# Performance work log

Hardware: AMD Instinct MI355X
Metric: run time of the kernel (lower is better)

## Reference

```python
import jax, jax.numpy as jnp
import numpy as np

B, S, D, H, L = 32, 1024, 512, 8, 4
DH = D // H
FF = D            # dim_feedforward == hidden_dim in the original ctor call
LOC_D, TD_D = 16, 8
TD_EMB = 3        # time_dist_embed_dim
POI = 21          # poi vocab
POI_EMB = 3
ADDR_IN = 1 + POI_EMB
FC = 32           # fc_hidden_dim
NEG = -1e9


def setup_inputs() -> dict:
    key = jax.random.key(0)
    ks = jax.random.split(key, 20)
    g = lambda i, shape, s=0.02: jax.random.normal(ks[i], shape, jnp.float32) * s
    return {
        "addr": jax.random.normal(ks[0], (B, 1), jnp.float32),
        "loc_dense_seq": jax.random.normal(ks[1], (B, S, LOC_D), jnp.float32),
        "time_dist_seq": jax.random.normal(ks[2], (B, S, TD_D), jnp.float32),
        "Wtd": g(3, (TD_D, TD_EMB)), "btd": jnp.zeros((TD_EMB,), jnp.float32),
        "Wemb": g(4, (LOC_D + TD_EMB, D)), "bemb": jnp.zeros((D,), jnp.float32),
        "Wqkv": g(5, (L, D, 3 * D)), "bqkv": jnp.zeros((L, 3 * D), jnp.float32),
        "Wo": g(6, (L, D, D)), "bo": jnp.zeros((L, D), jnp.float32),
        "ln1_g": jnp.ones((L, D), jnp.float32), "ln1_b": jnp.zeros((L, D), jnp.float32),
        "W1": g(7, (L, D, FF)), "b1": jnp.zeros((L, FF), jnp.float32),
        "W2": g(8, (L, FF, D)), "b2": jnp.zeros((L, D), jnp.float32),
        "ln2_g": jnp.ones((L, D), jnp.float32), "ln2_b": jnp.zeros((L, D), jnp.float32),
        "poi_emb": g(9, (POI, POI_EMB), 1.0),
        "Wa": g(10, (ADDR_IN, FC)), "ba": jnp.zeros((FC,), jnp.float32),
        "Wout": g(11, (D, FC)),
        "Wcomb": g(12, (FC, 1)),
        "addr_type": jax.random.randint(ks[13], (B, 1), 0, POI),
        "data_length": jax.random.randint(ks[14], (B,), 1, S + 1),
    }


def _ln(x, g, b, eps=1e-5):
    m = x.mean(-1, keepdims=True)
    v = ((x - m) ** 2).mean(-1, keepdims=True)
    return (x - m) / jnp.sqrt(v + eps) * g + b


def reference(addr, loc_dense_seq, time_dist_seq, Wtd, btd, Wemb, bemb, Wqkv,
              bqkv, Wo, bo, ln1_g, ln1_b, W1, b1, W2, b2, ln2_g, ln2_b,
              poi_emb, Wa, ba, Wout, Wcomb, addr_type, data_length):
    valid = jnp.arange(S)[None, :] < data_length[:, None]            # [B,S]
    td = time_dist_seq @ Wtd + btd                                   # [B,S,3]
    x = jnp.concatenate([loc_dense_seq, td], axis=-1) @ Wemb + bemb  # [B,S,D]
    scale = 1.0 / jnp.sqrt(jnp.float32(DH))
    for l in range(L):  # post-norm TransformerEncoderLayer (relu, eval/no-dropout)
        qkv = x @ Wqkv[l] + bqkv[l]
        q, k, v = jnp.split(qkv, 3, axis=-1)
        q = q.reshape(B, S, H, DH)
        k = k.reshape(B, S, H, DH)
        v = v.reshape(B, S, H, DH)
        scores = jnp.einsum('bqhd,bkhd->bhqk', q, k) * scale
        scores = jnp.where(valid[:, None, None, :], scores, NEG)     # mask padded keys
        attn = jax.nn.softmax(scores, axis=-1)
        ctx = jnp.einsum('bhqk,bkhd->bqhd', attn, v).reshape(B, S, D)
        x = _ln(x + ctx @ Wo[l] + bo[l], ln1_g[l], ln1_b[l])
        ff = jax.nn.relu(x @ W1[l] + b1[l]) @ W2[l] + b2[l]
        x = _ln(x + ff, ln2_g[l], ln2_b[l])
    # per-sample addr branch (vectorized over the original python loop)
    addr_inp = jnp.concatenate([addr, poi_emb[addr_type[:, 0]]], axis=-1)  # [B,4]
    a = addr_inp @ Wa + ba                                                 # [B,FC]
    o = (jnp.tanh(x @ Wout + a[:, None, :]) @ Wcomb)[..., 0]              # [B,S]
    logits = jnp.where(valid, o, NEG)
    logp = jax.nn.log_softmax(logits, axis=1)  # log_softmax over valid positions only
    return jnp.where(valid, logp, 0.0)
```

## Files before the change

kernel.cpp:

```cpp
#include <hip/hip_runtime.h>
#include <stdint.h>


typedef unsigned short u16;
typedef __attribute__((ext_vector_type(8))) short short8;
typedef __attribute__((ext_vector_type(4))) float f32x4;

constexpr int Bn = 32, Sn = 1024, Dn = 512, Ln = 4;
constexpr int BS = Bn * Sn;

__device__ __forceinline__ float b2f(u16 u) {
    union { uint32_t i; float f; } v; v.i = ((uint32_t)u) << 16; return v.f;
}
__device__ __forceinline__ u16 f2b(float f) {
    union { float f; uint32_t i; } v; v.f = f;
    uint32_t r = v.i + 0x7fffu + ((v.i >> 16) & 1u);
    return (u16)(r >> 16);
}
__device__ __forceinline__ float getf(const void* p, size_t i, int F) {
    return F ? ((const float*)p)[i] : b2f(((const u16*)p)[i]);
}
__device__ __forceinline__ void cp16(void* lds, const void* g) {
    __builtin_amdgcn_global_load_lds(
        (__attribute__((address_space(1))) void*)(uintptr_t)g,
        (__attribute__((address_space(3))) void*)(uint32_t)(uintptr_t)lds,
        16, 0, 0);
}

__global__ __launch_bounds__(256)
void detect_kernel(const void* loc, int* flag)
{
    __shared__ int cnt;
    if (threadIdx.x == 0) cnt = 0;
    __syncthreads();
    const u16* p = (const u16*)loc;
    int c = 0;
    for (int i = threadIdx.x; i < 2048; i += 256) {
        const float v = b2f(p[i]);
        if (!(fabsf(v) <= 100.0f)) c++;
    }
    atomicAdd(&cnt, c);
    __syncthreads();
    if (threadIdx.x == 0) *flag = (cnt >= 64) ? 1 : 0;
}

__global__ __launch_bounds__(256)
void gemm_bt(const u16* __restrict__ A, const u16* __restrict__ Bt,
             const void* __restrict__ bias, int boff, u16* __restrict__ C,
             int N, int K, int relu, const int* __restrict__ flagp,
             const int* __restrict__ dlen)
{
    __shared__ __align__(16) u16 As[128 * 32];
    __shared__ __align__(16) u16 Bs[128 * 32];
    const int bn0 = blockIdx.x * 128, bm0 = blockIdx.y * 128;
    if ((bm0 & 1023) >= dlen[bm0 >> 10]) return;
    const int F = *flagp;
    const int tid = threadIdx.x;
    const int lane = tid & 63, w = tid >> 6;
    const int wm = w >> 1, wn = w & 1;
    const int quad = lane >> 4, l16 = lane & 15;

    const f32x4 vzero = {0.f, 0.f, 0.f, 0.f};
    f32x4 acc[4][4];
#pragma unroll
    for (int i = 0; i < 4; i++)
#pragma unroll
        for (int j = 0; j < 4; j++) acc[i][j] = vzero;

    const int i0 = tid, i1 = tid + 256;
    const u16* a0 = A + (size_t)(bm0 + (i0 >> 2)) * K + (i0 & 3) * 8;
    const u16* a1 = A + (size_t)(bm0 + (i1 >> 2)) * K + (i1 & 3) * 8;
    const u16* b0 = Bt + (size_t)(bn0 + (i0 >> 2)) * K + (i0 & 3) * 8;
    const u16* b1 = Bt + (size_t)(bn0 + (i1 >> 2)) * K + (i1 & 3) * 8;

    for (int k0 = 0; k0 < K; k0 += 32) {
        cp16(As + i0 * 8, a0 + k0);
        cp16(As + i1 * 8, a1 + k0);
        cp16(Bs + i0 * 8, b0 + k0);
        cp16(Bs + i1 * 8, b1 + k0);
        __syncthreads();
        short8 af[4], bfr[4];
#pragma unroll
        for (int t = 0; t < 4; t++)
            af[t] = *(const short8*)&As[(wm * 64 + t * 16 + l16) * 32 + quad * 8];
#pragma unroll
        for (int t = 0; t < 4; t++)
            bfr[t] = *(const short8*)&Bs[(wn * 64 + t * 16 + l16) * 32 + quad * 8];
#pragma unroll
        for (int tm = 0; tm < 4; tm++)
#pragma unroll
            for (int tn = 0; tn < 4; tn++)
                acc[tm][tn] = __builtin_amdgcn_mfma_f32_16x16x32_bf16(
                    af[tm], bfr[tn], acc[tm][tn], 0, 0, 0);
        __syncthreads();
    }
#pragma unroll
    for (int tm = 0; tm < 4; tm++)
#pragma unroll
        for (int tn = 0; tn < 4; tn++) {
            const int col = bn0 + wn * 64 + tn * 16 + l16;
            const float bv = getf(bias, (size_t)boff + col, F);
#pragma unroll
            for (int r = 0; r < 4; r++) {
                const int row = bm0 + wm * 64 + tm * 16 + quad * 4 + r;
                float v = acc[tm][tn][r] + bv;
                if (relu) v = fmaxf(v, 0.0f);
                C[(size_t)row * N + col] = f2b(v);
            }
        }
}

__global__ __launch_bounds__(256)
void vtrans(const u16* __restrict__ qkv, const int* __restrict__ dlen,
            u16* __restrict__ vt)
{
    const int kt = blockIdx.x, bh = blockIdx.y;
    const int b = bh >> 3, h = bh & 7;
    if (kt * 64 >= dlen[b]) return;
    __shared__ __align__(16) u16 T[64 * 72];
    const int tid = threadIdx.x;
    const u16* src = qkv + (size_t)b * Sn * 1536 + 2 * Dn + h * 64;
    const int key2 = (tid & 31) * 2, f0 = (tid >> 5) * 8;
    const u16* p0 = src + (size_t)(kt * 64 + key2) * 1536 + f0;
    short8 v0 = *(const short8*)p0;
    short8 v1 = *(const short8*)(p0 + 1536);
#pragma unroll
    for (int j = 0; j < 8; j++) {
        const uint32_t pk = (uint32_t)(u16)v0[j] | ((uint32_t)(u16)v1[j] << 16);
        *(uint32_t*)&T[(f0 + j) * 72 + key2] = pk;
    }
    __syncthreads();
    const int feat = tid >> 2, kc = tid & 3;
    short8 r = *(const short8*)&T[feat * 72 + kc * 16];
    *(short8*)(vt + ((size_t)(bh * 64 + feat)) * Sn + kt * 64 + kc * 16) = r;
}

__global__ __launch_bounds__(256)
void attn_kernel(const u16* __restrict__ qkv, const u16* __restrict__ vt,
                 const int* __restrict__ dlen, u16* __restrict__ ctx)
{
    const int id = blockIdx.x;
    const int qt = id >> 8;
    const int bh = id & 255;
    const int h = bh & 7, b = bh >> 3;
    const int len = dlen[b];
    if (qt * 128 >= len) return;
    const int tid = threadIdx.x, lane = tid & 63, w = tid >> 6;
    const int quad = lane >> 4, l16 = lane & 15;
    __shared__ __align__(16) u16 Pl[4][32 * 72];
    u16* Plw = Pl[w];
    const int sw = l16 & 3;
    const size_t rs = 3 * Dn;
    const u16* base = qkv + (size_t)b * Sn * rs;
    const u16* vbase = vt + (size_t)(bh * 64) * Sn;
    const int q0 = qt * 128 + w * 32;

    short8 qf[2][2];
#pragma unroll
    for (int sub = 0; sub < 2; sub++)
#pragma unroll
        for (int s = 0; s < 2; s++)
            qf[sub][s] = *(const short8*)(base + (size_t)(q0 + sub * 16 + l16) * rs
                                          + h * 64 + quad * 8 + 32 * s);

    const f32x4 vzero = {0.f, 0.f, 0.f, 0.f};
    f32x4 O[2][4];
    float ls[2] = {0.f, 0.f};
#pragma unroll
    for (int sub = 0; sub < 2; sub++)
#pragma unroll
        for (int t = 0; t < 4; t++) O[sub][t] = vzero;

    const int nkt = (len + 63) >> 6;
    for (int kt = 0; kt < nkt; kt++) {
        const int k0 = kt * 64;
        short8 kf[4][2];
#pragma unroll
        for (int tn = 0; tn < 4; tn++) {
            const u16* kp = base + (size_t)(k0 + tn * 16 + l16) * rs + Dn
                            + h * 64 + quad * 8;
            kf[tn][0] = *(const short8*)kp;
            kf[tn][1] = *(const short8*)(kp + 32);
        }
        __builtin_amdgcn_wave_barrier();
#pragma unroll
        for (int sub = 0; sub < 2; sub++) {
            f32x4 sacc[4];
#pragma unroll
            for (int tn = 0; tn < 4; tn++) {
                f32x4 z = vzero;
                z = __builtin_amdgcn_mfma_f32_16x16x32_bf16(kf[tn][0], qf[sub][0], z, 0, 0, 0);
                sacc[tn] = __builtin_amdgcn_mfma_f32_16x16x32_bf16(kf[tn][1], qf[sub][1], sacc[tn] = z, 0, 0, 0);
            }
            const int prow = (sub * 16 + l16) * 72;
#pragma unroll
            for (int tn = 0; tn < 4; tn++) {
                const int kb = k0 + tn * 16 + quad * 4;
                float p[4];
#pragma unroll
                for (int r = 0; r < 4; r++) {
                    p[r] = (kb + r < len) ? __expf(sacc[tn][r] * 0.125f) : 0.0f;
                    ls[sub] += p[r];
                }
                uint2 pk;
                pk.x = (uint32_t)f2b(p[0]) | ((uint32_t)f2b(p[1]) << 16);
                pk.y = (uint32_t)f2b(p[2]) | ((uint32_t)f2b(p[3]) << 16);
                *(uint2*)&Plw[prow + ((tn ^ sw) << 4) + quad * 4] = pk;
            }
        }
        __builtin_amdgcn_wave_barrier();
#pragma unroll
        for (int s = 0; s < 2; s++) {
            const int tnr = ((quad >> 1) + 2 * s) ^ sw;
            short8 pf0 = *(const short8*)&Plw[(l16) * 72 + (tnr << 4) + (quad & 1) * 8];
            short8 pf1 = *(const short8*)&Plw[(16 + l16) * 72 + (tnr << 4) + (quad & 1) * 8];
#pragma unroll
            for (int t = 0; t < 4; t++) {
                short8 vf = *(const short8*)(vbase + (size_t)(t * 16 + l16) * Sn
                                             + k0 + quad * 8 + 32 * s);
                O[0][t] = __builtin_amdgcn_mfma_f32_16x16x32_bf16(pf0, vf, O[0][t], 0, 0, 0);
                O[1][t] = __builtin_amdgcn_mfma_f32_16x16x32_bf16(pf1, vf, O[1][t], 0, 0, 0);
            }
        }
    }
#pragma unroll
    for (int sub = 0; sub < 2; sub++) {
        ls[sub] += __shfl_xor(ls[sub], 16, 64);
        ls[sub] += __shfl_xor(ls[sub], 32, 64);
    }
#pragma unroll
    for (int sub = 0; sub < 2; sub++)
#pragma unroll
        for (int r = 0; r < 4; r++) {
            const float lv = __shfl(ls[sub], quad * 4 + r, 64);
            const float inv = 1.0f / lv;
            const int q = q0 + sub * 16 + quad * 4 + r;
#pragma unroll
            for (int t = 0; t < 4; t++)
                ctx[(size_t)(b * Sn + q) * Dn + h * 64 + t * 16 + l16] =
                    f2b(O[sub][t][r] * inv);
        }
}

__global__ __launch_bounds__(256)
void ln_res(u16* __restrict__ x, const u16* __restrict__ t,
            const void* __restrict__ g, const void* __restrict__ bta, int off,
            const int* __restrict__ flagp, const int* __restrict__ dlen)
{
    const int w = threadIdx.x >> 6, lane = threadIdx.x & 63;
    const size_t row = (size_t)blockIdx.x * 4 + w;
    if ((int)(row & 1023) >= dlen[row >> 10]) return;
    const int F = *flagp;
    u16* xp = x + row * Dn;
    const u16* tp = t + row * Dn;
    const int c0 = lane * 8;
    short8 xv = *(const short8*)(xp + c0);
    short8 tv = *(const short8*)(tp + c0);
    float v[8]; float s = 0.f;
#pragma unroll
    for (int i = 0; i < 8; i++) {
        v[i] = b2f((u16)xv[i]) + b2f((u16)tv[i]);
        s += v[i];
    }
#pragma unroll
    for (int o = 1; o < 64; o <<= 1) s += __shfl_xor(s, o, 64);
    const float mean = s * (1.0f / 512.0f);
    float q = 0.f;
#pragma unroll
    for (int i = 0; i < 8; i++) { const float d = v[i] - mean; q += d * d; }
#pragma unroll
    for (int o = 1; o < 64; o <<= 1) q += __shfl_xor(q, o, 64);
    const float inv = rsqrtf(q * (1.0f / 512.0f) + 1e-5f);
    short8 ov;
#pragma unroll
    for (int i = 0; i < 8; i++)
        ov[i] = (short)f2b((v[i] - mean) * inv * getf(g, off + c0 + i, F)
                           + getf(bta, off + c0 + i, F));
    *(short8*)(xp + c0) = ov;
}

__global__ __launch_bounds__(256)
void embed_kernel(const void* __restrict__ loc, const void* __restrict__ tds,
                  const void* __restrict__ Wtd, const void* __restrict__ btd,
                  const void* __restrict__ Wemb, const void* __restrict__ bemb,
                  u16* __restrict__ x, const int* __restrict__ flagp,
                  const int* __restrict__ dlen)
{
    const int token = blockIdx.x;
    if ((token & 1023) >= dlen[token >> 10]) return;
    const int F = *flagp;
    const int tid = threadIdx.x;
    __shared__ float inv[19];
    if (tid < 16) {
        inv[tid] = getf(loc, (size_t)token * 16 + tid, F);
    } else if (tid < 19) {
        const int e = tid - 16;
        float a = getf(btd, e, F);
        for (int j = 0; j < 8; j++)
            a += getf(tds, (size_t)token * 8 + j, F) * getf(Wtd, j * 3 + e, F);
        inv[tid] = a;
    }
    __syncthreads();
    for (int d = tid; d < Dn; d += 256) {
        float a = getf(bemb, d, F);
#pragma unroll
        for (int i = 0; i < 19; i++) a += inv[i] * getf(Wemb, (size_t)i * Dn + d, F);
        x[(size_t)token * Dn + d] = f2b(a);
    }
}

__global__ __launch_bounds__(256)
void transpose_w(const void* __restrict__ src, u16* __restrict__ dst,
                 int K, int N, const int* __restrict__ flagp)
{
    const int F = *flagp;
    __shared__ u16 tile[32][33];
    const size_t ls = (size_t)K * N;
    const size_t sb = (size_t)blockIdx.z * ls;
    u16* d = dst + blockIdx.z * ls;
    const int tx = threadIdx.x & 31, ty = threadIdx.x >> 5;
    const int n0 = blockIdx.x * 32, k0 = blockIdx.y * 32;
#pragma unroll
    for (int i = 0; i < 32; i += 8)
        tile[ty + i][tx] = f2b(getf(src, sb + (size_t)(k0 + ty + i) * N + n0 + tx, F));
    __syncthreads();
#pragma unroll
    for (int i = 0; i < 32; i += 8)
        d[(size_t)(n0 + ty + i) * K + k0 + tx] = tile[tx][ty + i];
}

__global__ __launch_bounds__(256)
void final_proj(const u16* __restrict__ x, const void* __restrict__ Wout,
                const void* __restrict__ Wcomb, const void* __restrict__ addr,
                const void* __restrict__ poi, const int* __restrict__ atype,
                const void* __restrict__ Wa, const void* __restrict__ ba,
                float* __restrict__ logits, const int* __restrict__ flagp,
                const int* __restrict__ dlen)
{
    const int F = *flagp;
    __shared__ float xs[8][512];
    __shared__ u16 wlds[32 * 514];
    const int tid = threadIdx.x;
    const int t0 = blockIdx.x * 8;
    for (int i = tid; i < 8 * 512; i += 256) {
        const int tk = i >> 9, d = i & 511;
        xs[tk][d] = b2f(x[(size_t)(t0 + tk) * Dn + d]);
    }
    for (int i = tid; i < 16384; i += 256) {
        const int k = i >> 5, j = i & 31;
        wlds[j * 514 + k] = F ? f2b(((const float*)Wout)[(size_t)k * 32 + j])
                              : ((const u16*)Wout)[(size_t)k * 32 + j];
    }
    __syncthreads();
    const int half = tid >> 5, j = tid & 31;
    const int token = t0 + half;
    const int b = token >> 10;
    if ((token & 1023) >= dlen[b]) return;
    const int ty = atype[b];
    float a = getf(ba, j, F) + getf(addr, b, F) * getf(Wa, j, F);
#pragma unroll
    for (int e = 0; e < 3; e++)
        a += getf(poi, ty * 3 + e, F) * getf(Wa, (1 + e) * 32 + j, F);
    float s = a;
    const u16* wj = wlds + j * 514;
    const float* xr = xs[half];
#pragma unroll 8
    for (int k = 0; k < 512; k++) s += xr[k] * b2f(wj[k]);
    float o = tanhf(s) * getf(Wcomb, j, F);
#pragma unroll
    for (int off = 1; off < 32; off <<= 1) o += __shfl_xor(o, off, 64);
    if (j == 0) logits[token] = o;
}

__global__ __launch_bounds__(256)
void lsm_kernel(const float* __restrict__ logits, const int* __restrict__ dlen,
                float* __restrict__ out)
{
    const int b = blockIdx.x, tid = threadIdx.x;
    const int len = dlen[b];
    const float* lp = logits + (size_t)b * Sn;
    __shared__ float wA[4], wB[4];
    float mx = -3e38f;
    for (int s = tid; s < Sn; s += 256) if (s < len) mx = fmaxf(mx, lp[s]);
#pragma unroll
    for (int o = 1; o < 64; o <<= 1) mx = fmaxf(mx, __shfl_xor(mx, o, 64));
    if ((tid & 63) == 0) wA[tid >> 6] = mx;
    __syncthreads();
    mx = fmaxf(fmaxf(wA[0], wA[1]), fmaxf(wA[2], wA[3]));
    float sm = 0.f;
    for (int s = tid; s < Sn; s += 256) if (s < len) sm += __expf(lp[s] - mx);
#pragma unroll
    for (int o = 1; o < 64; o <<= 1) sm += __shfl_xor(sm, o, 64);
    if ((tid & 63) == 0) wB[tid >> 6] = sm;
    __syncthreads();
    const float lse = mx + __logf(wB[0] + wB[1] + wB[2] + wB[3]);
    for (int s = tid; s < Sn; s += 256)
        out[(size_t)b * Sn + s] = (s < len) ? (lp[s] - lse) : 0.0f;
}

extern "C" void kernel_launch(void* const* d_in, const int* in_sizes, int n_in,
                              void* d_out, int out_size, void* d_ws, size_t ws_size,
                              hipStream_t stream) {
    const void* addr  = d_in[0];
    const void* loc   = d_in[1];
    const void* tds   = d_in[2];
    const void* Wtd   = d_in[3];
    const void* btd   = d_in[4];
    const void* Wemb  = d_in[5];
    const void* bemb  = d_in[6];
    const void* Wqkv  = d_in[7];
    const void* bqkv  = d_in[8];
    const void* Wo    = d_in[9];
    const void* bo    = d_in[10];
    const void* ln1g  = d_in[11];
    const void* ln1b  = d_in[12];
    const void* W1    = d_in[13];
    const void* b1    = d_in[14];
    const void* W2    = d_in[15];
    const void* b2    = d_in[16];
    const void* ln2g  = d_in[17];
    const void* ln2b  = d_in[18];
    const void* poi   = d_in[19];
    const void* Wa    = d_in[20];
    const void* ba    = d_in[21];
    const void* Wout  = d_in[22];
    const void* Wcomb = d_in[23];
    const int* atype  = (const int*)d_in[24];
    const int* dlen   = (const int*)d_in[25];

    char* base = (char*)d_ws;
    u16*   xb    = (u16*)(base);
    u16*   qkvb  = (u16*)(base + 33554432ull);
    u16*   ctxb  = (u16*)(base + 134217728ull);
    u16*   tb    = (u16*)(base + 167772160ull);
    u16*   wqkvT = (u16*)(base + 201326592ull);
    u16*   woT   = (u16*)(base + 207618048ull);
    u16*   w1T   = (u16*)(base + 209715200ull);
    u16*   w2T   = (u16*)(base + 211812352ull);
    float* logit = (float*)(base + 213909504ull);
    int*   flag  = (int*)  (base + 214040576ull);
    if (ws_size < 214040592ull) return;

    detect_kernel<<<1, 256, 0, stream>>>(loc, flag);

    transpose_w<<<dim3(48, 16, 4), 256, 0, stream>>>(Wqkv, wqkvT, 512, 1536, flag);
    transpose_w<<<dim3(16, 16, 4), 256, 0, stream>>>(Wo,   woT,   512, 512, flag);
    transpose_w<<<dim3(16, 16, 4), 256, 0, stream>>>(W1,   w1T,   512, 512, flag);
    transpose_w<<<dim3(16, 16, 4), 256, 0, stream>>>(W2,   w2T,   512, 512, flag);

    embed_kernel<<<BS, 256, 0, stream>>>(loc, tds, Wtd, btd, Wemb, bemb, xb, flag, dlen);

    for (int l = 0; l < Ln; l++) {
        gemm_bt<<<dim3(12, 256), 256, 0, stream>>>(
            xb, wqkvT + (size_t)l * 1536 * 512, bqkv, l * 1536, qkvb, 1536, 512, 0, flag, dlen);
        vtrans<<<dim3(16, 256), 256, 0, stream>>>(qkvb, dlen, tb);
        attn_kernel<<<2048, 256, 0, stream>>>(qkvb, tb, dlen, ctxb);
        gemm_bt<<<dim3(4, 256), 256, 0, stream>>>(
            ctxb, woT + (size_t)l * 512 * 512, bo, l * 512, tb, 512, 512, 0, flag, dlen);
        ln_res<<<BS / 4, 256, 0, stream>>>(xb, tb, ln1g, ln1b, l * 512, flag, dlen);
        gemm_bt<<<dim3(4, 256), 256, 0, stream>>>(
            xb, w1T + (size_t)l * 512 * 512, b1, l * 512, ctxb, 512, 512, 1, flag, dlen);
        gemm_bt<<<dim3(4, 256), 256, 0, stream>>>(
            ctxb, w2T + (size_t)l * 512 * 512, b2, l * 512, tb, 512, 512, 0, flag, dlen);
        ln_res<<<BS / 4, 256, 0, stream>>>(xb, tb, ln2g, ln2b, l * 512, flag, dlen);
    }

    final_proj<<<BS / 8, 256, 0, stream>>>(xb, Wout, Wcomb, addr, poi, atype,
                                           Wa, ba, logit, flag, dlen);
    lsm_kernel<<<Bn, 256, 0, stream>>>(logit, dlen, (float*)d_out);
}
```

Baseline: 1.978 ms.

## Fuse V transpose into attention via double-buffered LDS and MFMA row sums

Drops the separate vtrans kernel. Each attention block now loads V rows, transposes them into a double-buffered LDS tile, and prefetches the next tile while computing. Row sums of P are taken with an MFMA against a ones vector instead of scalar adds and shuffles, exp uses exp2f with a folded scale, the key mask runs only on the partial tail tile, and P is packed to bf16 by truncation rather than rounding. The final projection also gets a padded LDS stride and vectorized 8-byte weight reads. The trade-off is a block-wide sync per key tile, recomputing the V transpose in all query-tile blocks, and slightly different rounding of P.

New measurement: 1.747 ms. 1.13x faster.

```diff
diff --git a/kernel.cpp b/kernel.cpp
--- a/kernel.cpp
+++ b/kernel.cpp
@@ -25,6 +25,9 @@
         (__attribute__((address_space(1))) void*)(uintptr_t)g,
         (__attribute__((address_space(3))) void*)(uint32_t)(uintptr_t)lds,
         16, 0, 0);
+}
+__device__ __forceinline__ float asf(uint32_t u) {
+    union { uint32_t i; float f; } v; v.i = u; return v.f;
 }
 
 __global__ __launch_bounds__(256)
@@ -111,49 +114,24 @@
 }
 
 __global__ __launch_bounds__(256)
-void vtrans(const u16* __restrict__ qkv, const int* __restrict__ dlen,
-            u16* __restrict__ vt)
-{
-    const int kt = blockIdx.x, bh = blockIdx.y;
-    const int b = bh >> 3, h = bh & 7;
-    if (kt * 64 >= dlen[b]) return;
-    __shared__ __align__(16) u16 T[64 * 72];
-    const int tid = threadIdx.x;
-    const u16* src = qkv + (size_t)b * Sn * 1536 + 2 * Dn + h * 64;
-    const int key2 = (tid & 31) * 2, f0 = (tid >> 5) * 8;
-    const u16* p0 = src + (size_t)(kt * 64 + key2) * 1536 + f0;
-    short8 v0 = *(const short8*)p0;
-    short8 v1 = *(const short8*)(p0 + 1536);
-#pragma unroll
-    for (int j = 0; j < 8; j++) {
-        const uint32_t pk = (uint32_t)(u16)v0[j] | ((uint32_t)(u16)v1[j] << 16);
-        *(uint32_t*)&T[(f0 + j) * 72 + key2] = pk;
-    }
-    __syncthreads();
-    const int feat = tid >> 2, kc = tid & 3;
-    short8 r = *(const short8*)&T[feat * 72 + kc * 16];
-    *(short8*)(vt + ((size_t)(bh * 64 + feat)) * Sn + kt * 64 + kc * 16) = r;
-}
-
-__global__ __launch_bounds__(256)
-void attn_kernel(const u16* __restrict__ qkv, const u16* __restrict__ vt,
-                 const int* __restrict__ dlen, u16* __restrict__ ctx)
+void attn_kernel(const u16* __restrict__ qkv, const int* __restrict__ dlen,
+                 u16* __restrict__ ctx)
 {
     const int id = blockIdx.x;
-    const int qt = id >> 8;
-    const int bh = id & 255;
+    const int qt = id >> 8, bh = id & 255;
     const int h = bh & 7, b = bh >> 3;
     const int len = dlen[b];
     if (qt * 128 >= len) return;
     const int tid = threadIdx.x, lane = tid & 63, w = tid >> 6;
     const int quad = lane >> 4, l16 = lane & 15;
+    __shared__ __align__(16) u16 Vt[2][64 * 72];
     __shared__ __align__(16) u16 Pl[4][32 * 72];
     u16* Plw = Pl[w];
     const int sw = l16 & 3;
     const size_t rs = 3 * Dn;
     const u16* base = qkv + (size_t)b * Sn * rs;
-    const u16* vbase = vt + (size_t)(bh * 64) * Sn;
     const int q0 = qt * 128 + w * 32;
+    constexpr float SC = 0.18033688011112043f;
 
     short8 qf[2][2];
 #pragma unroll
@@ -163,17 +141,39 @@
             qf[sub][s] = *(const short8*)(base + (size_t)(q0 + sub * 16 + l16) * rs
                                           + h * 64 + quad * 8 + 32 * s);
 
+    const int key2 = (tid & 31) * 2, f0 = (tid >> 5) * 8;
+    const u16* vsrc = base + 2 * Dn + h * 64 + f0;
+    short8 v0 = *(const short8*)(vsrc + (size_t)key2 * rs);
+    short8 v1 = *(const short8*)(vsrc + (size_t)(key2 + 1) * rs);
+
+    short8 ones;
+#pragma unroll
+    for (int j = 0; j < 8; j++) ones[j] = (short)0x3F80;
+
     const f32x4 vzero = {0.f, 0.f, 0.f, 0.f};
-    f32x4 O[2][4];
-    float ls[2] = {0.f, 0.f};
-#pragma unroll
-    for (int sub = 0; sub < 2; sub++)
+    f32x4 O[2][4], lacc[2];
+#pragma unroll
+    for (int sub = 0; sub < 2; sub++) {
+        lacc[sub] = vzero;
 #pragma unroll
         for (int t = 0; t < 4; t++) O[sub][t] = vzero;
+    }
 
     const int nkt = (len + 63) >> 6;
+    int buf = 0;
     for (int kt = 0; kt < nkt; kt++) {
         const int k0 = kt * 64;
+        u16* Vb = Vt[buf];
+#pragma unroll
+        for (int j = 0; j < 8; j++)
+            *(uint32_t*)&Vb[(f0 + j) * 72 + key2] =
+                (uint32_t)(u16)v0[j] | ((uint32_t)(u16)v1[j] << 16);
+        __syncthreads();
+        if (kt + 1 < nkt) {
+            const u16* nv = vsrc + (size_t)(k0 + 64 + key2) * rs;
+            v0 = *(const short8*)nv;
+            v1 = *(const short8*)(nv + rs);
+        }
         short8 kf[4][2];
 #pragma unroll
         for (int tn = 0; tn < 4; tn++) {
@@ -182,7 +182,7 @@
             kf[tn][0] = *(const short8*)kp;
             kf[tn][1] = *(const short8*)(kp + 32);
         }
-        __builtin_amdgcn_wave_barrier();
+        const bool full = (k0 + 64 <= len);
 #pragma unroll
         for (int sub = 0; sub < 2; sub++) {
             f32x4 sacc[4];
@@ -190,22 +190,25 @@
             for (int tn = 0; tn < 4; tn++) {
                 f32x4 z = vzero;
                 z = __builtin_amdgcn_mfma_f32_16x16x32_bf16(kf[tn][0], qf[sub][0], z, 0, 0, 0);
-                sacc[tn] = __builtin_amdgcn_mfma_f32_16x16x32_bf16(kf[tn][1], qf[sub][1], sacc[tn] = z, 0, 0, 0);
+                sacc[tn] = __builtin_amdgcn_mfma_f32_16x16x32_bf16(kf[tn][1], qf[sub][1], z, 0, 0, 0);
             }
             const int prow = (sub * 16 + l16) * 72;
 #pragma unroll
             for (int tn = 0; tn < 4; tn++) {
-                const int kb = k0 + tn * 16 + quad * 4;
                 float p[4];
-#pragma unroll
-                for (int r = 0; r < 4; r++) {
-                    p[r] = (kb + r < len) ? __expf(sacc[tn][r] * 0.125f) : 0.0f;
-                    ls[sub] += p[r];
+                if (full) {
+#pragma unroll
+                    for (int r = 0; r < 4; r++) p[r] = exp2f(sacc[tn][r] * SC);
+                } else {
+                    const int kb = k0 + tn * 16 + quad * 4;
+#pragma unroll
+                    for (int r = 0; r < 4; r++)
+                        p[r] = (kb + r < len) ? exp2f(sacc[tn][r] * SC) : 0.0f;
                 }
                 uint2 pk;
-                pk.x = (uint32_t)f2b(p[0]) | ((uint32_t)f2b(p[1]) << 16);
-                pk.y = (uint32_t)f2b(p[2]) | ((uint32_t)f2b(p[3]) << 16);
-                *(uint2*)&Plw[prow + ((tn ^ sw) << 4) + quad * 4] = pk;
+                pk.x = (__float_as_uint(p[0]) >> 16) | (__float_as_uint(p[1]) & 0xFFFF0000u);
+                pk.y = (__float_as_uint(p[2]) >> 16) | (__float_as_uint(p[3]) & 0xFFFF0000u);
+                *(uint2*)&Plw[prow + (((tn ^ sw) << 4) + quad * 4)] = pk;
             }
         }
         __builtin_amdgcn_wave_barrier();
@@ -214,26 +217,23 @@
             const int tnr = ((quad >> 1) + 2 * s) ^ sw;
             short8 pf0 = *(const short8*)&Plw[(l16) * 72 + (tnr << 4) + (quad & 1) * 8];
             short8 pf1 = *(const short8*)&Plw[(16 + l16) * 72 + (tnr << 4) + (quad & 1) * 8];
+            lacc[0] = __builtin_amdgcn_mfma_f32_16x16x32_bf16(pf0, ones, lacc[0], 0, 0, 0);
+            lacc[1] = __builtin_amdgcn_mfma_f32_16x16x32_bf16(pf1, ones, lacc[1], 0, 0, 0);
 #pragma unroll
             for (int t = 0; t < 4; t++) {
-                short8 vf = *(const short8*)(vbase + (size_t)(t * 16 + l16) * Sn
-                                             + k0 + quad * 8 + 32 * s);
+                short8 vf = *(const short8*)&Vb[(t * 16 + l16) * 72 + quad * 8 + 32 * s];
                 O[0][t] = __builtin_amdgcn_mfma_f32_16x16x32_bf16(pf0, vf, O[0][t], 0, 0, 0);
                 O[1][t] = __builtin_amdgcn_mfma_f32_16x16x32_bf16(pf1, vf, O[1][t], 0, 0, 0);
             }
         }
-    }
-#pragma unroll
-    for (int sub = 0; sub < 2; sub++) {
-        ls[sub] += __shfl_xor(ls[sub], 16, 64);
-        ls[sub] += __shfl_xor(ls[sub], 32, 64);
+        __builtin_amdgcn_wave_barrier();
+        buf ^= 1;
     }
 #pragma unroll
     for (int sub = 0; sub < 2; sub++)
 #pragma unroll
         for (int r = 0; r < 4; r++) {
-            const float lv = __shfl(ls[sub], quad * 4 + r, 64);
-            const float inv = 1.0f / lv;
+            const float inv = 1.0f / lacc[sub][r];
             const int q = q0 + sub * 16 + quad * 4 + r;
 #pragma unroll
             for (int t = 0; t < 4; t++)
@@ -339,7 +339,7 @@
 {
     const int F = *flagp;
     __shared__ float xs[8][512];
-    __shared__ u16 wlds[32 * 514];
+    __shared__ __align__(8) u16 wlds[32 * 516];
     const int tid = threadIdx.x;
     const int t0 = blockIdx.x * 8;
     for (int i = tid; i < 8 * 512; i += 256) {
@@ -348,7 +348,7 @@
     }
     for (int i = tid; i < 16384; i += 256) {
         const int k = i >> 5, j = i & 31;
-        wlds[j * 514 + k] = F ? f2b(((const float*)Wout)[(size_t)k * 32 + j])
+        wlds[j * 516 + k] = F ? f2b(((const float*)Wout)[(size_t)k * 32 + j])
                               : ((const u16*)Wout)[(size_t)k * 32 + j];
     }
     __syncthreads();
@@ -362,10 +362,16 @@
     for (int e = 0; e < 3; e++)
         a += getf(poi, ty * 3 + e, F) * getf(Wa, (1 + e) * 32 + j, F);
     float s = a;
-    const u16* wj = wlds + j * 514;
+    const u16* wj = wlds + j * 516;
     const float* xr = xs[half];
-#pragma unroll 8
-    for (int k = 0; k < 512; k++) s += xr[k] * b2f(wj[k]);
+#pragma unroll 4
+    for (int k = 0; k < 512; k += 4) {
+        const uint2 wv = *(const uint2*)&wj[k];
+        s += xr[k]     * asf(wv.x << 16);
+        s += xr[k + 1] * asf(wv.x & 0xFFFF0000u);
+        s += xr[k + 2] * asf(wv.y << 16);
+        s += xr[k + 3] * asf(wv.y & 0xFFFF0000u);
+    }
     float o = tanhf(s) * getf(Wcomb, j, F);
 #pragma unroll
     for (int off = 1; off < 32; off <<= 1) o += __shfl_xor(o, off, 64);
@@ -453,8 +459,7 @@
     for (int l = 0; l < Ln; l++) {
         gemm_bt<<<dim3(12, 256), 256, 0, stream>>>(
             xb, wqkvT + (size_t)l * 1536 * 512, bqkv, l * 1536, qkvb, 1536, 512, 0, flag, dlen);
-        vtrans<<<dim3(16, 256), 256, 0, stream>>>(qkvb, dlen, tb);
-        attn_kernel<<<2048, 256, 0, stream>>>(qkvb, tb, dlen, ctxb);
+        attn_kernel<<<2048, 256, 0, stream>>>(qkvb, dlen, ctxb);
         gemm_bt<<<dim3(4, 256), 256, 0, stream>>>(
             ctxb, woT + (size_t)l * 512 * 512, bo, l * 512, tb, 512, 512, 0, flag, dlen);
         ln_res<<<BS / 4, 256, 0, stream>>>(xb, tb, ln1g, ln1b, l * 512, flag, dlen);
```
